# Kernel tuning notes

Hardware: AMD Instinct MI355X
Metric: run time of the kernel (lower is better)

## Reference

```python
import jax, jax.numpy as jnp
import numpy as np
from jax.scipy.special import logsumexp

EPS = 1e-6
SINKHORN_ITERS = 8
TEMPERATURE = 1.0


def sinkhorn(logits):
    # log(clamp(t, min=eps)) / temperature, then alternating row/col log-normalization
    t = jnp.log(jnp.clip(logits, EPS)) / TEMPERATURE
    for _ in range(SINKHORN_ITERS):
        t = t - logsumexp(t, axis=-2, keepdims=True)  # over tokens n
        t = t - logsumexp(t, axis=-1, keepdims=True)  # over experts e
    return jnp.exp(t)


def setup_inputs() -> dict:
    key = jax.random.key(0)
    k1, k2, k3 = jax.random.split(key, 3)
    b, n, d, e, h = 4, 4096, 1024, 8, 1
    x = jax.random.normal(k1, (b, n, d), dtype=jnp.float32)
    gate_w = jax.random.normal(k2, (h, d, e), dtype=jnp.float32)  # to_gate_weight
    experts = jax.random.normal(k3, (e, d, d), dtype=jnp.float32) * 0.02  # expert weight tensor [e, i, o]
    return {"x": x, "gate_w": gate_w, "experts": experts}


def reference(x, gate_w, experts):
    b, n, d = x.shape
    h, _, e = gate_w.shape
    m = n // e  # tokens_per_expert

    xh = x[:, None]  # b 1 n d  (single-headed path)

    # gate logits: b h n e
    gate_logits = jnp.einsum('bhnd,hde->bhne', xh, gate_w)

    # competitive sinkhorn gates (eval mode, no gumbel noise)
    gates = sinkhorn(gate_logits)

    # topk over token dim (dim=-2) with k = tokens_per_expert
    g = jnp.swapaxes(gates, -1, -2)          # b h e n
    gv, idx = jax.lax.top_k(g, m)            # b h e m
    gate_values = jnp.swapaxes(gv, -1, -2)   # b h m e
    routed_indices = jnp.swapaxes(idx, -1, -2)  # b h m e

    # eval + competitive -> hard gates
    hard_gates = (gate_values > 0.5).astype(x.dtype)  # b h m e

    # gather routed tokens: routed[b,h,m,e,d] = x[b,h,idx[b,h,m,e],d]
    bi = jnp.arange(b)[:, None, None, None]
    hi = jnp.arange(h)[None, :, None, None]
    routed = xh[bi, hi, routed_indices]  # b h m e d

    # per-expert GEMM, vectorized over experts: experts [e,i,o] -> [e,h,i,o]
    experts4 = experts[:, None, :, :]
    out = jnp.einsum('bhmei,ehio->bhmeo', routed, experts4)  # b h m e o

    # weight by gates
    out = out * hard_gates[..., None]

    # scatter back (set semantics, as in einx set_at)
    y = jnp.zeros_like(xh).at[bi, hi, routed_indices].set(out)  # b h n d
    return y[:, 0]  # b n d
```

## Files before the change

### kernel.cpp

```cpp
#include <hip/hip_runtime.h>
#include <hip/hip_bf16.h>
#include <stdint.h>

#define BB 4
#define NN 4096
#define DD 1024
#define EE 8
#define MM 512
#define BN (BB*NN)

#define SBLK 32
#define SPB  8
#define SROWS 512

#define FRONT_GATE 512
#define FRONT_CONV 2048
#define FRONT_INIT 64
#define FRONT_BLKS (FRONT_GATE + FRONT_CONV + FRONT_INIT)

typedef __bf16 bf16x8 __attribute__((ext_vector_type(8)));
typedef float  floatx4 __attribute__((ext_vector_type(4)));

typedef const __attribute__((address_space(1))) void* gptr_t;
typedef __attribute__((address_space(3))) void* lptr_t;

__device__ __forceinline__ unsigned short f2bf(float f) {
    union { float f; unsigned u; } v; v.f = f;
    unsigned r = v.u + 0x7fffu + ((v.u >> 16) & 1u);
    return (unsigned short)(r >> 16);
}

__device__ __forceinline__ float gate_reduce8(const float acc[8], int lane) {
    float k1[4];
#pragma unroll
    for (int e = 0; e < 4; e++) {
        float a = acc[e]     + __shfl_xor(acc[e],     1, 64);
        float b = acc[e + 4] + __shfl_xor(acc[e + 4], 1, 64);
        k1[e] = (lane & 1) ? b : a;
    }
    float k2[2];
#pragma unroll
    for (int e = 0; e < 2; e++) {
        float a = k1[e]     + __shfl_xor(k1[e],     2, 64);
        float b = k1[e + 2] + __shfl_xor(k1[e + 2], 2, 64);
        k2[e] = (lane & 2) ? b : a;
    }
    float a = k2[0] + __shfl_xor(k2[0], 4, 64);
    float b = k2[1] + __shfl_xor(k2[1], 4, 64);
    float v = (lane & 4) ? b : a;
    v += __shfl_xor(v, 8, 64);
    v += __shfl_xor(v, 16, 64);
    v += __shfl_xor(v, 32, 64);
    return v;
}

#define OFF_GATES   0u
#define OFF_TOPK    524288u
#define OFF_WIN     589824u
#define OFF_COUNTS  655360u
#define OFF_LISTS   655616u
#define OFF_FLAGS   721152u
#define OFF_PART    737536u
#define OFF_KEYS    753920u
#define OFF_XBF     1802496u
#define OFF_EXPT    35356928u
#define WS_NEEDED   52134144u

__global__ __launch_bounds__(256, 2) void front_kernel(const float* __restrict__ x,
                                                       const float* __restrict__ gw,
                                                       const float* __restrict__ E,
                                                       float* __restrict__ tmat,
                                                       unsigned short* __restrict__ xbf,
                                                       unsigned short* __restrict__ expt,
                                                       int* __restrict__ win,
                                                       int* __restrict__ counts,
                                                       unsigned* __restrict__ flags) {
    __shared__ float tile[64][65];
    int bid = blockIdx.x;
    int tid = threadIdx.x;

    if (bid < FRONT_GATE) {
        int wave = tid >> 6, lane = tid & 63;
        float4 g0[4][4], g1[4][4];
#pragma unroll
        for (int j = 0; j < 4; j++)
#pragma unroll
            for (int r = 0; r < 4; r++) {
                const float4* p = (const float4*)(gw + (size_t)(j * 256 + lane * 4 + r) * 8);
                g0[j][r] = p[0];
                g1[j][r] = p[1];
            }
        int tok0 = (bid * 4 + wave) * 8;
        int exp_id = ((lane & 1) << 2) | (lane & 2) | ((lane & 4) >> 2);
        for (int tt = 0; tt < 8; tt += 2) {
            int tokA = tok0 + tt, tokB = tokA + 1;
            const float4* xrA = (const float4*)(x + (size_t)tokA * DD);
            const float4* xrB = (const float4*)(x + (size_t)tokB * DD);
            float4 xa[4], xc[4];
#pragma unroll
            for (int j = 0; j < 4; j++) xa[j] = xrA[j * 64 + lane];
#pragma unroll
            for (int j = 0; j < 4; j++) xc[j] = xrB[j * 64 + lane];
            if (xbf) {
#pragma unroll
                for (int j = 0; j < 4; j++) {
                    ushort4 o;
                    o.x = f2bf(xa[j].x); o.y = f2bf(xa[j].y); o.z = f2bf(xa[j].z); o.w = f2bf(xa[j].w);
                    ((ushort4*)(xbf + (size_t)tokA * DD))[j * 64 + lane] = o;
                }
#pragma unroll
                for (int j = 0; j < 4; j++) {
                    ushort4 o;
                    o.x = f2bf(xc[j].x); o.y = f2bf(xc[j].y); o.z = f2bf(xc[j].z); o.w = f2bf(xc[j].w);
                    ((ushort4*)(xbf + (size_t)tokB * DD))[j * 64 + lane] = o;
                }
            }
            float accA[8] = {0.f, 0.f, 0.f, 0.f, 0.f, 0.f, 0.f, 0.f};
            float accB[8] = {0.f, 0.f, 0.f, 0.f, 0.f, 0.f, 0.f, 0.f};
#pragma unroll
            for (int j = 0; j < 4; j++) {
                accA[0] += xa[j].x * g0[j][0].x + xa[j].y * g0[j][1].x + xa[j].z * g0[j][2].x + xa[j].w * g0[j][3].x;
                accA[1] += xa[j].x * g0[j][0].y + xa[j].y * g0[j][1].y + xa[j].z * g0[j][2].y + xa[j].w * g0[j][3].y;
                accA[2] += xa[j].x * g0[j][0].z + xa[j].y * g0[j][1].z + xa[j].z * g0[j][2].z + xa[j].w * g0[j][3].z;
                accA[3] += xa[j].x * g0[j][0].w + xa[j].y * g0[j][1].w + xa[j].z * g0[j][2].w + xa[j].w * g0[j][3].w;
                accA[4] += xa[j].x * g1[j][0].x + xa[j].y * g1[j][1].x + xa[j].z * g1[j][2].x + xa[j].w * g1[j][3].x;
                accA[5] += xa[j].x * g1[j][0].y + xa[j].y * g1[j][1].y + xa[j].z * g1[j][2].y + xa[j].w * g1[j][3].y;
                accA[6] += xa[j].x * g1[j][0].z + xa[j].y * g1[j][1].z + xa[j].z * g1[j][2].z + xa[j].w * g1[j][3].z;
                accA[7] += xa[j].x * g1[j][0].w + xa[j].y * g1[j][1].w + xa[j].z * g1[j][2].w + xa[j].w * g1[j][3].w;
                accB[0] += xc[j].x * g0[j][0].x + xc[j].y * g0[j][1].x + xc[j].z * g0[j][2].x + xc[j].w * g0[j][3].x;
                accB[1] += xc[j].x * g0[j][0].y + xc[j].y * g0[j][1].y + xc[j].z * g0[j][2].y + xc[j].w * g0[j][3].y;
                accB[2] += xc[j].x * g0[j][0].z + xc[j].y * g0[j][1].z + xc[j].z * g0[j][2].z + xc[j].w * g0[j][3].z;
                accB[3] += xc[j].x * g0[j][0].w + xc[j].y * g0[j][1].w + xc[j].z * g0[j][2].w + xc[j].w * g0[j][3].w;
                accB[4] += xc[j].x * g1[j][0].x + xc[j].y * g1[j][1].x + xc[j].z * g1[j][2].x + xc[j].w * g1[j][3].x;
                accB[5] += xc[j].x * g1[j][0].y + xc[j].y * g1[j][1].y + xc[j].z * g1[j][2].y + xc[j].w * g1[j][3].y;
                accB[6] += xc[j].x * g1[j][0].z + xc[j].y * g1[j][1].z + xc[j].z * g1[j][2].z + xc[j].w * g1[j][3].z;
                accB[7] += xc[j].x * g1[j][0].w + xc[j].y * g1[j][1].w + xc[j].z * g1[j][2].w + xc[j].w * g1[j][3].w;
            }
            float vA = gate_reduce8(accA, lane);
            float vB = gate_reduce8(accB, lane);
            if (lane < 8) {
                tmat[(size_t)tokA * EE + exp_id] = logf(fmaxf(vA, 1e-6f));
                tmat[(size_t)tokB * EE + exp_id] = logf(fmaxf(vB, 1e-6f));
            }
        }
    } else if (bid < FRONT_GATE + FRONT_CONV) {
        if (!expt) return;
        int cb = bid - FRONT_GATE;
        int e = cb >> 8, t = cb & 255;
        int k0 = (t >> 4) * 64, c0 = (t & 15) * 64;
#pragma unroll
        for (int ii = 0; ii < 4; ii++) {
            int r = (tid >> 4) + ii * 16;
            int c4 = (tid & 15) * 4;
            float4 v = *(const float4*)(E + ((size_t)e * DD + k0 + r) * DD + c0 + c4);
            tile[r][c4 + 0] = v.x; tile[r][c4 + 1] = v.y; tile[r][c4 + 2] = v.z; tile[r][c4 + 3] = v.w;
        }
        __syncthreads();
        int cc = tid >> 2, kk0 = (tid & 3) * 16;
#pragma unroll
        for (int q = 0; q < 4; q++) {
            ushort4 o;
            o.x = f2bf(tile[kk0 + q * 4 + 0][cc]);
            o.y = f2bf(tile[kk0 + q * 4 + 1][cc]);
            o.z = f2bf(tile[kk0 + q * 4 + 2][cc]);
            o.w = f2bf(tile[kk0 + q * 4 + 3][cc]);
            *(ushort4*)&expt[((size_t)e * DD + c0 + cc) * DD + k0 + kk0 + q * 4] = o;
        }
    } else {
        int i = (bid - FRONT_GATE - FRONT_CONV) * 256 + tid;
        win[i] = -1;
        if (i < 32) counts[i] = 0;
        if (i < 4096) flags[i] = 0u;
    }
}

__global__ __launch_bounds__(512) void sinkhorn_mb(const float* __restrict__ tmat,
                                                   float* __restrict__ part,
                                                   unsigned* __restrict__ flags,
                                                   unsigned long long* __restrict__ keys) {
    int g = blockIdx.x;
    int b = g >> 3, sl = g & 7;
    int tid = threadIdx.x;
    int wave = tid >> 6, lane = tid & 63;
    int row = sl * SROWS + tid;
    const float* tr = tmat + ((size_t)b * NN + row) * EE;
    float tv[EE];
#pragma unroll
    for (int e = 0; e < EE; e++) tv[e] = tr[e];

    __shared__ float red[8][8];
    __shared__ float bcm[8];

    for (int it = 0; it < 8; it++) {
#pragma unroll
        for (int e = 0; e < EE; e++) {
            float s = expf(tv[e]);
            for (int off = 32; off > 0; off >>= 1) s += __shfl_down(s, off, 64);
            if (lane == 0) red[wave][e] = s;
        }
        __syncthreads();
        if (tid == 0) {
            float* pm = part + (size_t)(it * 32 + b * 8 + sl) * 16;
#pragma unroll
            for (int e = 0; e < EE; e++) {
                float s = 0.f;
#pragma unroll
                for (int w = 0; w < 8; w++) s += red[w][e];
                __hip_atomic_store(&pm[e], s, __ATOMIC_RELAXED, __HIP_MEMORY_SCOPE_AGENT);
            }
            __hip_atomic_store(&flags[(size_t)(it * 32 + b * 8 + sl) * 16], 1u,
                               __ATOMIC_RELEASE, __HIP_MEMORY_SCOPE_AGENT);
        }
        if (tid < 8) {
            const unsigned* f = flags + (size_t)(it * 32 + b * 8 + tid) * 16;
            while (__hip_atomic_load(f, __ATOMIC_ACQUIRE, __HIP_MEMORY_SCOPE_AGENT) == 0u)
                __builtin_amdgcn_s_sleep(1);
        }
        __syncthreads();
        if (tid < 8) {
            const float* pb = part + (size_t)(it * 32 + b * 8) * 16;
            float s = 0.f;
#pragma unroll
            for (int p = 0; p < SPB; p++)
                s += __hip_atomic_load(&pb[p * 16 + tid], __ATOMIC_RELAXED, __HIP_MEMORY_SCOPE_AGENT);
            bcm[tid] = logf(s);
        }
        __syncthreads();
#pragma unroll
        for (int e = 0; e < EE; e++) tv[e] -= bcm[e];
        {
            float s = 0.f;
#pragma unroll
            for (int e = 0; e < EE; e++) s += expf(tv[e]);
            float lse = logf(s);
#pragma unroll
            for (int e = 0; e < EE; e++) tv[e] -= lse;
        }
    }
#pragma unroll
    for (int e = 0; e < EE; e++) {
        unsigned fb = __float_as_uint(expf(tv[e]));
        keys[(size_t)(b * EE + e) * NN + row] =
            ((unsigned long long)fb << 32) | (unsigned)(~row);
    }
}

__global__ __launch_bounds__(256) void rank_topk_kernel(const unsigned long long* __restrict__ keys,
                                                        float* __restrict__ topk_val,
                                                        int* __restrict__ win) {
    int be = blockIdx.y;
    int b = be >> 3, e = be & 7;
    int tid = threadIdx.x;
    int t = blockIdx.x * 256 + tid;
    const unsigned long long* kcol = keys + (size_t)be * NN;
    unsigned long long my = kcol[t];

    unsigned long long kb[16];
#pragma unroll
    for (int i = 0; i < 16; i++) kb[i] = kcol[i];

    int c0 = 0, c1 = 0, c2 = 0, c3 = 0;
    for (int j = 0; j < NN - 16; j += 16) {
        unsigned long long kn[16];
#pragma unroll
        for (int i = 0; i < 16; i++) kn[i] = kcol[j + 16 + i];
#pragma unroll
        for (int i = 0; i < 16; i += 4) {
            c0 += (int)(kb[i + 0] > my);
            c1 += (int)(kb[i + 1] > my);
            c2 += (int)(kb[i + 2] > my);
            c3 += (int)(kb[i + 3] > my);
        }
#pragma unroll
        for (int i = 0; i < 16; i++) kb[i] = kn[i];
    }
#pragma unroll
    for (int i = 0; i < 16; i += 4) {
        c0 += (int)(kb[i + 0] > my);
        c1 += (int)(kb[i + 1] > my);
        c2 += (int)(kb[i + 2] > my);
        c3 += (int)(kb[i + 3] > my);
    }
    int cnt = (c0 + c1) + (c2 + c3);
    if (cnt < MM) {
        topk_val[be * MM + cnt] = __uint_as_float((unsigned)(my >> 32));
        atomicMax(&win[b * NN + t], cnt * 8 + e);
    }
}

__global__ __launch_bounds__(256) void build_zero_kernel(const float* __restrict__ topk_val,
                                                         const int* __restrict__ win,
                                                         int* __restrict__ counts,
                                                         int* __restrict__ lists,
                                                         float* __restrict__ y) {
    __shared__ int act_s[64];
    int base = blockIdx.x * 64;
    int tid = threadIdx.x;
    if (tid < 64) {
        int i = base + tid;
        int b = i >> 12, tok = i & 4095;
        int w = win[i];
        int active = 0;
        if (w >= 0) {
            int m = w >> 3, e = w & 7;
            float gv = topk_val[(b * 8 + e) * MM + m];
            if (gv > 0.5f) {
                int p = atomicAdd(&counts[b * 8 + e], 1);
                lists[(b * 8 + e) * MM + p] = tok;
                active = 1;
            }
        }
        act_s[tid] = active;
    }
    __syncthreads();
    float4 z = make_float4(0.f, 0.f, 0.f, 0.f);
    for (int r = 0; r < 64; r++) {
        if (!act_s[r])
            ((float4*)(y + (size_t)(base + r) * DD))[tid] = z;
    }
}

__global__ __launch_bounds__(256) void expert_gemm_mfma(const unsigned short* __restrict__ xbf,
                                                        const unsigned short* __restrict__ expt,
                                                        const int* __restrict__ counts,
                                                        const int* __restrict__ lists,
                                                        float* __restrict__ y) {
    int be = blockIdx.z;
    int b = be >> 3, e = be & 7;
    int cnt = counts[be];
    int row0 = blockIdx.y * 64;
    if (row0 >= cnt) return;
    int col0 = blockIdx.x * 128;

    __shared__ unsigned short As[64 * 32];
    __shared__ unsigned short Bs[128 * 32];
    __shared__ int toks[64];

    int tid = threadIdx.x;
    int wave = tid >> 6, lane = tid & 63;
    int m16 = lane & 15, quad = lane >> 4;
    int wave_m = wave >> 1, wave_n = wave & 1;

    if (tid < 64) {
        int r = row0 + tid;
        toks[tid] = lists[be * MM + (r < cnt ? r : cnt - 1)];
    }

    int r0 = tid >> 2;
    int ch = tid & 3;

    const unsigned short* xb = xbf + (size_t)b * NN * DD;
    const unsigned short* Eb = expt + (size_t)e * DD * DD;

    floatx4 acc[2][4];
#pragma unroll
    for (int i = 0; i < 2; i++)
#pragma unroll
        for (int j = 0; j < 4; j++) acc[i][j] = (floatx4)0.f;

    for (int k0 = 0; k0 < DD; k0 += 32) {
        __syncthreads();
        {
            const unsigned short* gA  = xb + (size_t)toks[r0] * DD + k0 + ch * 8;
            const unsigned short* gB0 = Eb + (size_t)(col0 + r0) * DD + k0 + ch * 8;
            const unsigned short* gB1 = Eb + (size_t)(col0 + 64 + r0) * DD + k0 + ch * 8;
            __builtin_amdgcn_global_load_lds((gptr_t)gA,  (lptr_t)(As + (size_t)tid * 8), 16, 0, 0);
            __builtin_amdgcn_global_load_lds((gptr_t)gB0, (lptr_t)(Bs + (size_t)tid * 8), 16, 0, 0);
            __builtin_amdgcn_global_load_lds((gptr_t)gB1, (lptr_t)(Bs + 64 * 32 + (size_t)tid * 8), 16, 0, 0);
        }
        __syncthreads();
        bf16x8 af[2], bfr[4];
#pragma unroll
        for (int i = 0; i < 2; i++)
            af[i] = *(const bf16x8*)&As[(wave_m * 32 + i * 16 + m16) * 32 + quad * 8];
#pragma unroll
        for (int j = 0; j < 4; j++)
            bfr[j] = *(const bf16x8*)&Bs[(wave_n * 64 + j * 16 + m16) * 32 + quad * 8];
#pragma unroll
        for (int i = 0; i < 2; i++)
#pragma unroll
            for (int j = 0; j < 4; j++)
                acc[i][j] = __builtin_amdgcn_mfma_f32_16x16x32_bf16(af[i], bfr[j], acc[i][j], 0, 0, 0);
    }

#pragma unroll
    for (int i = 0; i < 2; i++) {
#pragma unroll
        for (int r = 0; r < 4; r++) {
            int lr = wave_m * 32 + i * 16 + quad * 4 + r;
            if (row0 + lr < cnt) {
                int tok = toks[lr];
                float* yr = y + ((size_t)b * NN + tok) * DD + col0 + wave_n * 64 + m16;
#pragma unroll
                for (int j = 0; j < 4; j++) yr[j * 16] = acc[i][j][r];
            }
        }
    }
}

__global__ __launch_bounds__(256) void expert_gemm_kernel(const float* __restrict__ x,
                                                          const float* __restrict__ experts,
                                                          const int* __restrict__ counts,
                                                          const int* __restrict__ lists,
                                                          float* __restrict__ y) {
    int be = blockIdx.z;
    int b = be >> 3, e = be & 7;
    int cnt = counts[be];
    int row0 = blockIdx.y * 64;
    if (row0 >= cnt) return;
    int col0 = blockIdx.x * 64;
    __shared__ float As2[16][68];
    __shared__ float Bs2[16][68];
    __shared__ int toks[64];
    int tid = threadIdx.x;
    if (tid < 64) {
        int r = row0 + tid;
        toks[tid] = (r < cnt) ? lists[be * MM + r] : -1;
    }
    __syncthreads();
    int tx = tid & 15, ty = tid >> 4;
    int ar = tid >> 2;
    int ak = (tid & 3) * 4;
    int bk = tid >> 4;
    int bc4 = (tid & 15) * 4;
    int atok = toks[ar];
    const float* xb = x + (size_t)b * NN * DD;
    const float* Eb = experts + (size_t)e * DD * DD + col0;
    float acc[4][4] = {};
    for (int k0 = 0; k0 < DD; k0 += 16) {
        float4 av;
        if (atok >= 0) av = *(const float4*)(xb + (size_t)atok * DD + k0 + ak);
        else av = make_float4(0.f, 0.f, 0.f, 0.f);
        float4 bv = *(const float4*)(Eb + (size_t)(k0 + bk) * DD + bc4);
        __syncthreads();
        As2[ak + 0][ar] = av.x; As2[ak + 1][ar] = av.y; As2[ak + 2][ar] = av.z; As2[ak + 3][ar] = av.w;
        *(float4*)&Bs2[bk][bc4] = bv;
        __syncthreads();
#pragma unroll
        for (int kk = 0; kk < 16; kk++) {
            float4 a = *(const float4*)&As2[kk][ty * 4];
            float4 bb = *(const float4*)&Bs2[kk][tx * 4];
            acc[0][0] += a.x * bb.x; acc[0][1] += a.x * bb.y; acc[0][2] += a.x * bb.z; acc[0][3] += a.x * bb.w;
            acc[1][0] += a.y * bb.x; acc[1][1] += a.y * bb.y; acc[1][2] += a.y * bb.z; acc[1][3] += a.y * bb.w;
            acc[2][0] += a.z * bb.x; acc[2][1] += a.z * bb.y; acc[2][2] += a.z * bb.z; acc[2][3] += a.z * bb.w;
            acc[3][0] += a.w * bb.x; acc[3][1] += a.w * bb.y; acc[3][2] += a.w * bb.z; acc[3][3] += a.w * bb.w;
        }
    }
#pragma unroll
    for (int i = 0; i < 4; i++) {
        int rl = ty * 4 + i;
        if (row0 + rl < cnt) {
            int tok = toks[rl];
            float4 o = make_float4(acc[i][0], acc[i][1], acc[i][2], acc[i][3]);
            *(float4*)(y + ((size_t)b * NN + tok) * DD + col0 + tx * 4) = o;
        }
    }
}

extern "C" void kernel_launch(void* const* d_in, const int* in_sizes, int n_in,
                              void* d_out, int out_size, void* d_ws, size_t ws_size,
                              hipStream_t stream) {
    const float* x       = (const float*)d_in[0];
    const float* gw      = (const float*)d_in[1];
    const float* experts = (const float*)d_in[2];
    float* y = (float*)d_out;

    char* ws = (char*)d_ws;
    float*    gates    = (float*)(ws + OFF_GATES);
    float*    topk_val = (float*)(ws + OFF_TOPK);
    int*      win      = (int*)(ws + OFF_WIN);
    int*      counts   = (int*)(ws + OFF_COUNTS);
    int*      lists    = (int*)(ws + OFF_LISTS);
    unsigned* flags    = (unsigned*)(ws + OFF_FLAGS);
    float*    part     = (float*)(ws + OFF_PART);
    unsigned long long* keys = (unsigned long long*)(ws + OFF_KEYS);
    bool big = ws_size >= WS_NEEDED;
    unsigned short* xbf  = big ? (unsigned short*)(ws + OFF_XBF)  : nullptr;
    unsigned short* expt = big ? (unsigned short*)(ws + OFF_EXPT) : nullptr;

    front_kernel<<<FRONT_BLKS, 256, 0, stream>>>(x, gw, experts, gates, xbf, expt,
                                                 win, counts, flags);
    sinkhorn_mb<<<SBLK, 512, 0, stream>>>(gates, part, flags, keys);
    rank_topk_kernel<<<dim3(16, 32), 256, 0, stream>>>(keys, topk_val, win);
    build_zero_kernel<<<256, 256, 0, stream>>>(topk_val, win, counts, lists, y);
    if (big)
        expert_gemm_mfma<<<dim3(8, 8, BB * EE), 256, 0, stream>>>(xbf, expt, counts, lists, y);
    else
        expert_gemm_kernel<<<dim3(16, 8, BB * EE), 256, 0, stream>>>(x, experts, counts, lists, y);
}
```

Measured before the change: 308.0 us.

## Split rank counting across key chunks with atomic adds, resolve winners in build

Rank counting for top-k is split four ways over key chunks along a new grid dimension. Each chunk adds its partial count into a rank array, which sinkhorn zeroes and which aliases the gates buffer. The per-token winner selection that used to happen with atomicMax during the rank pass now happens in build_zero by scanning all eight experts' ranks, and the gate value is read straight from the keys. This gives the serial O(N) comparison loop four times more parallelism, at the cost of extra atomics and extra rank reads.

```diff
diff --git a/kernel.cpp b/kernel.cpp
--- a/kernel.cpp
+++ b/kernel.cpp
@@ -72,7 +72,6 @@
                                                        float* __restrict__ tmat,
                                                        unsigned short* __restrict__ xbf,
                                                        unsigned short* __restrict__ expt,
-                                                       int* __restrict__ win,
                                                        int* __restrict__ counts,
                                                        unsigned* __restrict__ flags) {
     __shared__ float tile[64][65];
@@ -168,7 +167,6 @@
         }
     } else {
         int i = (bid - FRONT_GATE - FRONT_CONV) * 256 + tid;
-        win[i] = -1;
         if (i < 32) counts[i] = 0;
         if (i < 4096) flags[i] = 0u;
     }
@@ -177,7 +175,8 @@
 __global__ __launch_bounds__(512) void sinkhorn_mb(const float* __restrict__ tmat,
                                                    float* __restrict__ part,
                                                    unsigned* __restrict__ flags,
-                                                   unsigned long long* __restrict__ keys) {
+                                                   unsigned long long* __restrict__ keys,
+                                                   int* __restrict__ rank) {
     int g = blockIdx.x;
     int b = g >> 3, sl = g & 7;
     int tid = threadIdx.x;
@@ -243,53 +242,38 @@
         keys[(size_t)(b * EE + e) * NN + row] =
             ((unsigned long long)fb << 32) | (unsigned)(~row);
     }
-}
-
-__global__ __launch_bounds__(256) void rank_topk_kernel(const unsigned long long* __restrict__ keys,
-                                                        float* __restrict__ topk_val,
-                                                        int* __restrict__ win) {
+    {
+        int4* rz = (int4*)(rank + (size_t)b * EE * NN) + (size_t)sl * (EE * NN / 8 / 4);
+        int4 z4 = make_int4(0, 0, 0, 0);
+        rz[tid * 2 + 0] = z4;
+        rz[tid * 2 + 1] = z4;
+    }
+}
+
+__global__ __launch_bounds__(256) void rank_count_kernel(const unsigned long long* __restrict__ keys,
+                                                         int* __restrict__ rank) {
     int be = blockIdx.y;
-    int b = be >> 3, e = be & 7;
     int tid = threadIdx.x;
     int t = blockIdx.x * 256 + tid;
     const unsigned long long* kcol = keys + (size_t)be * NN;
     unsigned long long my = kcol[t];
-
-    unsigned long long kb[16];
-#pragma unroll
-    for (int i = 0; i < 16; i++) kb[i] = kcol[i];
+    const unsigned long long* ks = kcol + (size_t)blockIdx.z * (NN / 4);
 
     int c0 = 0, c1 = 0, c2 = 0, c3 = 0;
-    for (int j = 0; j < NN - 16; j += 16) {
-        unsigned long long kn[16];
-#pragma unroll
-        for (int i = 0; i < 16; i++) kn[i] = kcol[j + 16 + i];
+    for (int j = 0; j < NN / 4; j += 16) {
 #pragma unroll
         for (int i = 0; i < 16; i += 4) {
-            c0 += (int)(kb[i + 0] > my);
-            c1 += (int)(kb[i + 1] > my);
-            c2 += (int)(kb[i + 2] > my);
-            c3 += (int)(kb[i + 3] > my);
-        }
-#pragma unroll
-        for (int i = 0; i < 16; i++) kb[i] = kn[i];
-    }
-#pragma unroll
-    for (int i = 0; i < 16; i += 4) {
-        c0 += (int)(kb[i + 0] > my);
-        c1 += (int)(kb[i + 1] > my);
-        c2 += (int)(kb[i + 2] > my);
-        c3 += (int)(kb[i + 3] > my);
-    }
-    int cnt = (c0 + c1) + (c2 + c3);
-    if (cnt < MM) {
-        topk_val[be * MM + cnt] = __uint_as_float((unsigned)(my >> 32));
-        atomicMax(&win[b * NN + t], cnt * 8 + e);
-    }
-}
-
-__global__ __launch_bounds__(256) void build_zero_kernel(const float* __restrict__ topk_val,
-                                                         const int* __restrict__ win,
+            c0 += (int)(ks[j + i + 0] > my);
+            c1 += (int)(ks[j + i + 1] > my);
+            c2 += (int)(ks[j + i + 2] > my);
+            c3 += (int)(ks[j + i + 3] > my);
+        }
+    }
+    atomicAdd(&rank[(size_t)be * NN + t], (c0 + c1) + (c2 + c3));
+}
+
+__global__ __launch_bounds__(256) void build_zero_kernel(const unsigned long long* __restrict__ keys,
+                                                         const int* __restrict__ rank,
                                                          int* __restrict__ counts,
                                                          int* __restrict__ lists,
                                                          float* __restrict__ y) {
@@ -299,14 +283,22 @@
     if (tid < 64) {
         int i = base + tid;
         int b = i >> 12, tok = i & 4095;
-        int w = win[i];
+        int wmax = -1;
+#pragma unroll
+        for (int e = 0; e < EE; e++) {
+            int r = rank[(size_t)(b * 8 + e) * NN + tok];
+            if (r < MM) {
+                int w = r * 8 + e;
+                wmax = wmax > w ? wmax : w;
+            }
+        }
         int active = 0;
-        if (w >= 0) {
-            int m = w >> 3, e = w & 7;
-            float gv = topk_val[(b * 8 + e) * MM + m];
-            if (gv > 0.5f) {
-                int p = atomicAdd(&counts[b * 8 + e], 1);
-                lists[(b * 8 + e) * MM + p] = tok;
+        if (wmax >= 0) {
+            int ew = wmax & 7;
+            unsigned hi = (unsigned)(keys[(size_t)(b * 8 + ew) * NN + tok] >> 32);
+            if (__uint_as_float(hi) > 0.5f) {
+                int p = atomicAdd(&counts[b * 8 + ew], 1);
+                lists[(b * 8 + ew) * MM + p] = tok;
                 active = 1;
             }
         }
@@ -467,8 +459,7 @@
 
     char* ws = (char*)d_ws;
     float*    gates    = (float*)(ws + OFF_GATES);
-    float*    topk_val = (float*)(ws + OFF_TOPK);
-    int*      win      = (int*)(ws + OFF_WIN);
+    int*      rank     = (int*)(ws + OFF_GATES);
     int*      counts   = (int*)(ws + OFF_COUNTS);
     int*      lists    = (int*)(ws + OFF_LISTS);
     unsigned* flags    = (unsigned*)(ws + OFF_FLAGS);
@@ -479,10 +470,10 @@
     unsigned short* expt = big ? (unsigned short*)(ws + OFF_EXPT) : nullptr;
 
     front_kernel<<<FRONT_BLKS, 256, 0, stream>>>(x, gw, experts, gates, xbf, expt,
-                                                 win, counts, flags);
-    sinkhorn_mb<<<SBLK, 512, 0, stream>>>(gates, part, flags, keys);
-    rank_topk_kernel<<<dim3(16, 32), 256, 0, stream>>>(keys, topk_val, win);
-    build_zero_kernel<<<256, 256, 0, stream>>>(topk_val, win, counts, lists, y);
+                                                 counts, flags);
+    sinkhorn_mb<<<SBLK, 512, 0, stream>>>(gates, part, flags, keys, rank);
+    rank_count_kernel<<<dim3(16, 32, 4), 256, 0, stream>>>(keys, rank);
+    build_zero_kernel<<<256, 256, 0, stream>>>(keys, rank, counts, lists, y);
     if (big)
         expert_gemm_mfma<<<dim3(8, 8, BB * EE), 256, 0, stream>>>(xbf, expt, counts, lists, y);
     else
```

Result: faster. 282.4 us (-8.3%).
